# Kernel optimization log

Measured on AMD Instinct MI355X. Metric: run time of the kernel, lower is better.

Reference implementation:

```python
import jax, jax.numpy as jnp
import numpy as np

D_MODEL = 2048
N_HEADS = 16
HEAD_DIM = D_MODEL // N_HEADS
ROPE_BASE = 10000.0
B, T = 2, 2048


def setup_inputs() -> dict:
    key = jax.random.key(0)
    k1, k2, k3 = jax.random.split(key, 3)
    s_in = 1.0 / np.sqrt(D_MODEL)
    x = jax.random.normal(k1, (B, T, D_MODEL), dtype=jnp.float32)
    Wqkv = jax.random.normal(k2, (3 * D_MODEL, D_MODEL), dtype=jnp.float32) * s_in
    bqkv = jnp.zeros((3 * D_MODEL,), dtype=jnp.float32)
    Wo = jax.random.normal(k3, (D_MODEL, D_MODEL), dtype=jnp.float32) * s_in
    bo = jnp.zeros((D_MODEL,), dtype=jnp.float32)
    return {"x": x, "Wqkv": Wqkv, "bqkv": bqkv, "Wo": Wo, "bo": bo}


def _rotate_half(x):
    # [x1,x2,x3,x4] -> [-x2,x1,-x4,x3] (interleaved pairs)
    x_even = x[..., 0::2]
    x_odd = x[..., 1::2]
    return jnp.stack((-x_odd, x_even), axis=-1).reshape(x.shape)


def _rope_cos_sin(seq_len, dtype):
    half = HEAD_DIM // 2
    inv_freq = 1.0 / (ROPE_BASE ** (jnp.arange(half, dtype=jnp.float32) / half))
    freqs = jnp.arange(seq_len, dtype=jnp.float32)[:, None] * inv_freq[None, :]  # (T, half)
    emb = jnp.repeat(freqs, 2, axis=-1)  # (T, D) interleaved
    cos = jnp.cos(emb).astype(dtype)[None, None]  # (1,1,T,D)
    sin = jnp.sin(emb).astype(dtype)[None, None]
    return cos, sin


def reference(x, Wqkv, bqkv, Wo, bo):
    b, t, c = x.shape
    qkv = jnp.einsum('btc,fc->btf', x, Wqkv) + bqkv  # (B,T,3C)
    q, k, v = jnp.split(qkv, 3, axis=-1)
    def to_heads(z):
        return z.reshape(b, t, N_HEADS, HEAD_DIM).transpose(0, 2, 1, 3)  # (B,H,T,D)
    q, k, v = to_heads(q), to_heads(k), to_heads(v)
    cos, sin = _rope_cos_sin(t, x.dtype)
    q = q * cos + _rotate_half(q) * sin
    k = k * cos + _rotate_half(k) * sin
    scale = 1.0 / jnp.sqrt(jnp.asarray(HEAD_DIM, dtype=x.dtype))
    scores = jnp.einsum('bhqd,bhkd->bhqk', q, k) * scale  # (B,H,T,T)
    causal = jnp.tril(jnp.ones((t, t), dtype=bool))
    scores = jnp.where(causal, scores, jnp.finfo(scores.dtype).min)
    attn = jax.nn.softmax(scores, axis=-1)
    out = jnp.einsum('bhqk,bhkd->bhqd', attn, v)  # (B,H,T,D)
    out = out.transpose(0, 2, 1, 3).reshape(b, t, c)
    return jnp.einsum('btc,oc->bto', out, Wo) + bo
```

## Files before the change

kernel.cpp:

```cpp
#include <hip/hip_runtime.h>

using f16 = _Float16;
typedef _Float16 h8 __attribute__((ext_vector_type(8)));
typedef _Float16 h4 __attribute__((ext_vector_type(4)));
typedef float f4 __attribute__((ext_vector_type(4)));
typedef unsigned int u32;
typedef unsigned long long u64;

#define DEVI static __device__ __forceinline__

DEVI f4 mfma16(h8 a, h8 b, f4 c) {
  return __builtin_amdgcn_mfma_f32_16x16x32_f16(a, b, c, 0, 0, 0);
}

DEVI void gl_lds16(const f16* g, f16* l) {
  __builtin_amdgcn_global_load_lds(
      (const __attribute__((address_space(1))) u32*)g,
      (__attribute__((address_space(3))) u32*)l, 16, 0, 0);
}

DEVI u32 pkh2(float a, float b) {
  union { f16 h[2]; u32 u; } x;
  x.h[0] = (f16)a; x.h[1] = (f16)b;
  return x.u;
}

typedef float fv4 __attribute__((ext_vector_type(4)));

__global__ __launch_bounds__(256) void k_cvt(const float* __restrict__ in,
                                             f16* __restrict__ out, int n4) {
  int i = blockIdx.x * 256 + threadIdx.x;
  if (i >= n4) return;
  fv4 v = ((const fv4*)in)[i];
  h4 o;
  o[0] = (f16)v[0]; o[1] = (f16)v[1]; o[2] = (f16)v[2]; o[3] = (f16)v[3];
  ((h4*)out)[i] = o;
}

__global__ __launch_bounds__(256) void k_rope_tbl(float* __restrict__ tbl) {
  int i = blockIdx.x * 256 + threadIdx.x;
  int t = i >> 6, d = i & 63;
  float invf = exp2f(-(float)d * (13.287712379549449f / 64.f));
  float a = (float)t * invf;
  tbl[2 * i]     = cosf(a);
  tbl[2 * i + 1] = sinf(a);
}

template <int F32OUT>
__global__ __launch_bounds__(256) void k_gemm_bt(const f16* __restrict__ A,
                                                 const f16* __restrict__ Bt,
                                                 const float* __restrict__ bias,
                                                 void* __restrict__ Cp,
                                                 int M, int N, int K) {
  __shared__ f16 lds[2 * 128 * 64];
  f16* sA = lds;
  f16* sB = lds + 128 * 64;
  const int tid = threadIdx.x;
  const int w = tid >> 6, lane = tid & 63;
  const int g = lane >> 4, colq = lane & 15;
  const int wr = w >> 1, wc = w & 1;
  const int bm = blockIdx.y, bn = blockIdx.x;

  f4 acc[4][4] = {};
  const int nk = K >> 6;
  const int lrow = lane >> 3;
  const int lch = lane & 7;

  for (int k0i = 0; k0i < nk; ++k0i) {
    const int k0 = k0i << 6;
#pragma unroll
    for (int c = 0; c < 4; ++c) {
      const int seg = c * 4 + w;
      const int row = seg * 8 + lrow;
      const f16* ga = A + (size_t)(bm * 128 + row) * K + k0 + lch * 8;
      const f16* gb = Bt + (size_t)(bn * 128 + row) * K + k0 + lch * 8;
      gl_lds16(ga, sA + seg * 512);
      gl_lds16(gb, sB + seg * 512);
    }
    __syncthreads();
#pragma unroll
    for (int kk = 0; kk < 64; kk += 32) {
      h8 af[4], bf[4];
#pragma unroll
      for (int m = 0; m < 4; ++m)
        af[m] = *(const h8*)(sA + (wr * 64 + m * 16 + colq) * 64 + kk + g * 8);
#pragma unroll
      for (int n = 0; n < 4; ++n)
        bf[n] = *(const h8*)(sB + (wc * 64 + n * 16 + colq) * 64 + kk + g * 8);
#pragma unroll
      for (int m = 0; m < 4; ++m)
#pragma unroll
        for (int n = 0; n < 4; ++n) acc[m][n] = mfma16(af[m], bf[n], acc[m][n]);
    }
    __syncthreads();
  }

#pragma unroll
  for (int n = 0; n < 4; ++n) {
    const int col = bn * 128 + wc * 64 + n * 16 + colq;
    const float bv = bias[col];
#pragma unroll
    for (int m = 0; m < 4; ++m) {
      const int row0 = bm * 128 + wr * 64 + m * 16 + 4 * g;
#pragma unroll
      for (int r = 0; r < 4; ++r) {
        float v = acc[m][n][r] + bv;
        if constexpr (F32OUT) {
          ((float*)Cp)[(size_t)(row0 + r) * N + col] = v;
        } else {
          ((f16*)Cp)[(size_t)(row0 + r) * N + col] = (f16)v;
        }
      }
    }
  }
}

__global__ __launch_bounds__(256) void k_rope(const f16* __restrict__ qkv,
                                              const float* __restrict__ tbl,
                                              f16* __restrict__ Q, f16* __restrict__ K) {
  int i = blockIdx.x * 256 + threadIdx.x;
  int d = i & 63;
  int h = (i >> 6) & 15;
  int bt = i >> 10;
  int t = bt & 2047;
  int bh = ((bt >> 11) << 4) | h;
  union { u32 u; f16 h2[2]; } qa, ka, qo, ko;
  qa.u = *(const u32*)(qkv + (size_t)bt * 6144 + h * 128 + 2 * d);
  ka.u = *(const u32*)(qkv + (size_t)bt * 6144 + 2048 + h * 128 + 2 * d);
  float c = tbl[2 * (t * 64 + d)];
  float s = tbl[2 * (t * 64 + d) + 1];
  float q0f = (float)qa.h2[0], q1f = (float)qa.h2[1];
  float k0f = (float)ka.h2[0], k1f = (float)ka.h2[1];
  const float SQ = 0.088388347648318447f * 1.4426950408889634f;
  qo.h2[0] = (f16)((q0f * c - q1f * s) * SQ);
  qo.h2[1] = (f16)((q1f * c + q0f * s) * SQ);
  ko.h2[0] = (f16)(k0f * c - k1f * s);
  ko.h2[1] = (f16)(k1f * c + k0f * s);
  *(u32*)(Q + ((size_t)bh * 2048 + t) * 128 + 2 * d) = qo.u;
  *(u32*)(K + ((size_t)bh * 2048 + t) * 128 + 2 * d) = ko.u;
}

__global__ __launch_bounds__(256) void k_vtrans(const f16* __restrict__ qkv,
                                                f16* __restrict__ Vt) {
  __shared__ f16 ldsT[128 * 40];
  const int bh = blockIdx.y, t0 = blockIdx.x * 32;
  const int b = bh >> 4, h = bh & 15;
  const int tid = threadIdx.x;
#pragma unroll
  for (int cc = 0; cc < 2; ++cc) {
    int task = tid + cc * 256;
    int row = task >> 4;
    int ch = task & 15;
    h8 v = *(const h8*)(qkv + (size_t)(b * 2048 + t0 + row) * 6144 + 4096 + h * 128 + ch * 8);
#pragma unroll
    for (int j = 0; j < 8; ++j) ldsT[(ch * 8 + j) * 40 + row] = v[j];
  }
  __syncthreads();
  int d = tid >> 1, seg = tid & 1;
  h8 v0 = *(const h8*)(ldsT + d * 40 + seg * 16);
  h8 v1 = *(const h8*)(ldsT + d * 40 + seg * 16 + 8);
  f16* dst = Vt + ((size_t)bh * 128 + d) * 2048 + t0 + seg * 16;
  *(h8*)dst = v0;
  *(h8*)(dst + 8) = v1;
}

DEVI void stage_tiles(const f16* __restrict__ Kg, const f16* __restrict__ Vtg,
                      f16* bufK, f16* bufV, int kv, int w, int lane) {
#pragma unroll
  for (int jj = 0; jj < 4; ++jj) {
    const int j = w * 4 + jj;
    const int rK = j * 4 + (lane >> 4);
    const int cK = (lane & 15) ^ ((rK & 7) << 1);
    gl_lds16(Kg + (size_t)(kv + rK) * 128 + cK * 8, bufK + j * 512);
    const int rV = j * 8 + (lane >> 3);
    const int cV = (lane & 7) ^ (rV & 7);
    gl_lds16(Vtg + (size_t)rV * 2048 + kv + cV * 8, bufV + j * 512);
  }
}

__global__ __launch_bounds__(256, 1) void k_attn(const f16* __restrict__ Q,
                                                 const f16* __restrict__ K,
                                                 const f16* __restrict__ Vt,
                                                 f16* __restrict__ O) {
  __shared__ f16 lds[2][16384];
  const int tid = threadIdx.x;
  const int w = tid >> 6, lane = tid & 63;
  const int g = lane >> 4, q = lane & 15;
  const int bid = blockIdx.x;
  const int bh = bid & 31;
  const int b = bid >> 5;

  const f16* Kg = K + (size_t)bh * 2048 * 128;
  const f16* Vtg = Vt + (size_t)bh * 128 * 2048;
  const int qx2 = (q & 7) << 1;
  const int qx = q & 7;

  for (int ph = 0; ph < 2; ++ph) {
    const int p = ph ? (15 - b) : b;
    const int q0w = p * 128 + w * 32;
    const int nit = 2 * (p + 1);

    h8 qf[2][4];
#pragma unroll
    for (int set = 0; set < 2; ++set)
#pragma unroll
      for (int d4 = 0; d4 < 4; ++d4)
        qf[set][d4] = *(const h8*)(Q + ((size_t)bh * 2048 + q0w + 16 * set + q) * 128 + d4 * 32 + g * 8);

    stage_tiles(Kg, Vtg, lds[0], lds[0] + 8192, 0, w, lane);
    asm volatile("s_waitcnt vmcnt(0)" ::: "memory");
    __builtin_amdgcn_s_barrier();

    f4 ot[2][8] = {};
    float mrun[2] = {-3.0e38f, -3.0e38f};
    float lrun[2] = {0.f, 0.f};

    for (int it = 0; it < nit; ++it) {
      const int kv0 = it * 64;
      f16* bufK = lds[it & 1];
      f16* bufV = bufK + 8192;
      if (it + 1 < nit) {
        f16* nb = lds[(it + 1) & 1];
        stage_tiles(Kg, Vtg, nb, nb + 8192, kv0 + 64, w, lane);
      }
      if (kv0 < q0w + 32) {
        f4 st[2][4] = {{{0.f,0.f,0.f,0.f},{0.f,0.f,0.f,0.f},{0.f,0.f,0.f,0.f},{0.f,0.f,0.f,0.f}},
                       {{0.f,0.f,0.f,0.f},{0.f,0.f,0.f,0.f},{0.f,0.f,0.f,0.f},{0.f,0.f,0.f,0.f}}};
#pragma unroll
        for (int d4 = 0; d4 < 4; ++d4) {
          h8 kf[4];
#pragma unroll
          for (int s = 0; s < 4; ++s)
            kf[s] = *(const h8*)(bufK + ((16 * s + q) * 16 + ((4 * d4 + g) ^ qx2)) * 8);
#pragma unroll
          for (int set = 0; set < 2; ++set)
#pragma unroll
            for (int s = 0; s < 4; ++s)
              st[set][s] = mfma16(kf[s], qf[set][d4], st[set][s]);
        }
        if (kv0 + 63 > q0w) {
#pragma unroll
          for (int set = 0; set < 2; ++set) {
            const int qcol = q0w + 16 * set + q;
#pragma unroll
            for (int s = 0; s < 4; ++s)
#pragma unroll
              for (int r = 0; r < 4; ++r)
                if (kv0 + s * 16 + 4 * g + r > qcol) st[set][s][r] = -3.0e38f;
          }
        }
        float pm[2];
#pragma unroll
        for (int set = 0; set < 2; ++set) {
          float m0 = st[set][0][0];
#pragma unroll
          for (int s = 0; s < 4; ++s)
#pragma unroll
            for (int r = 0; r < 4; ++r) m0 = fmaxf(m0, st[set][s][r]);
          m0 = fmaxf(m0, __shfl_xor(m0, 16));
          m0 = fmaxf(m0, __shfl_xor(m0, 32));
          pm[set] = m0;
        }
        const bool ok = (pm[0] <= mrun[0] + 8.0f) && (pm[1] <= mrun[1] + 8.0f);
        if (!__all(ok)) {
#pragma unroll
          for (int set = 0; set < 2; ++set) {
            float mnew = fmaxf(mrun[set], pm[set]);
            float corr = exp2f(mrun[set] - mnew);
            lrun[set] *= corr;
#pragma unroll
            for (int dt = 0; dt < 8; ++dt) ot[set][dt] *= corr;
            mrun[set] = mnew;
          }
        }
#pragma unroll
        for (int set = 0; set < 2; ++set) {
          float ps = 0.f;
#pragma unroll
          for (int s = 0; s < 4; ++s)
#pragma unroll
            for (int r = 0; r < 4; ++r) {
              st[set][s][r] = exp2f(st[set][s][r] - mrun[set]);
              ps += st[set][s][r];
            }
          ps += __shfl_xor(ps, 16);
          ps += __shfl_xor(ps, 32);
          lrun[set] += ps;
        }
        union { u32 u[4]; h8 h; } pb[2][2];
        const int s0l = ((g & 1) << 5) | q;
        const bool hi = g >= 2;
#pragma unroll
        for (int set = 0; set < 2; ++set)
#pragma unroll
          for (int hh = 0; hh < 2; ++hh) {
            u32 wA0 = pkh2(st[set][2 * hh][0], st[set][2 * hh][1]);
            u32 wB0 = pkh2(st[set][2 * hh][2], st[set][2 * hh][3]);
            u32 wA1 = pkh2(st[set][2 * hh + 1][0], st[set][2 * hh + 1][1]);
            u32 wB1 = pkh2(st[set][2 * hh + 1][2], st[set][2 * hh + 1][3]);
            u32 a0 = (u32)__shfl((int)wA0, s0l),      a1 = (u32)__shfl((int)wA1, s0l);
            u32 b0 = (u32)__shfl((int)wB0, s0l),      b1 = (u32)__shfl((int)wB1, s0l);
            u32 c0 = (u32)__shfl((int)wA0, s0l + 16), c1 = (u32)__shfl((int)wA1, s0l + 16);
            u32 d0 = (u32)__shfl((int)wB0, s0l + 16), d1 = (u32)__shfl((int)wB1, s0l + 16);
            pb[set][hh].u[0] = hi ? a1 : a0;
            pb[set][hh].u[1] = hi ? b1 : b0;
            pb[set][hh].u[2] = hi ? c1 : c0;
            pb[set][hh].u[3] = hi ? d1 : d0;
          }
#pragma unroll
        for (int hh = 0; hh < 2; ++hh)
#pragma unroll
          for (int dt = 0; dt < 8; ++dt) {
            h8 vf = *(const h8*)(bufV + ((dt * 16 + q) * 8 + ((4 * hh + g) ^ qx)) * 8);
#pragma unroll
            for (int set = 0; set < 2; ++set)
              ot[set][dt] = mfma16(vf, pb[set][hh].h, ot[set][dt]);
          }
      }
      asm volatile("s_waitcnt vmcnt(0)" ::: "memory");
      __builtin_amdgcn_s_barrier();
    }

#pragma unroll
    for (int set = 0; set < 2; ++set) {
      float linv = 1.0f / lrun[set];
      f16* Ob = O + ((size_t)(bh >> 4) * 2048 + q0w + 16 * set + q) * 2048 + (bh & 15) * 128 + 4 * g;
#pragma unroll
      for (int dt = 0; dt < 8; ++dt) {
        union { f16 hh4[4]; u64 u; } o;
#pragma unroll
        for (int r = 0; r < 4; ++r) o.hh4[r] = (f16)(ot[set][dt][r] * linv);
        *(u64*)(Ob + dt * 16) = o.u;
      }
    }
  }
}

extern "C" void kernel_launch(void* const* d_in, const int* in_sizes, int n_in,
                              void* d_out, int out_size, void* d_ws, size_t ws_size,
                              hipStream_t stream) {
  (void)in_sizes; (void)n_in; (void)out_size; (void)ws_size;
  const float* x    = (const float*)d_in[0];
  const float* Wqkv = (const float*)d_in[1];
  const float* bqkv = (const float*)d_in[2];
  const float* Wo   = (const float*)d_in[3];
  const float* bo   = (const float*)d_in[4];

  char* ws = (char*)d_ws;
  f16* xb    = (f16*)ws; ws += (size_t)4096 * 2048 * 2;
  f16* wqkvb = (f16*)ws; ws += (size_t)6144 * 2048 * 2;
  f16* wob   = (f16*)ws; ws += (size_t)2048 * 2048 * 2;
  f16* qkvb  = (f16*)ws; ws += (size_t)4096 * 6144 * 2;
  f16* Qb    = (f16*)ws; ws += (size_t)32 * 2048 * 128 * 2;
  f16* Kb    = (f16*)ws; ws += (size_t)32 * 2048 * 128 * 2;
  f16* Vtb   = (f16*)ws; ws += (size_t)32 * 128 * 2048 * 2;
  f16* attb  = (f16*)ws; ws += (size_t)4096 * 2048 * 2;
  float* tbl = (float*)ws; ws += (size_t)2048 * 64 * 2 * 4;

  k_cvt<<<8192, 256, 0, stream>>>(x, xb, 2097152);
  k_cvt<<<12288, 256, 0, stream>>>(Wqkv, wqkvb, 3145728);
  k_cvt<<<4096, 256, 0, stream>>>(Wo, wob, 1048576);
  k_rope_tbl<<<512, 256, 0, stream>>>(tbl);

  k_gemm_bt<0><<<dim3(48, 32), 256, 0, stream>>>(xb, wqkvb, bqkv, qkvb, 4096, 6144, 2048);

  k_rope<<<16384, 256, 0, stream>>>(qkvb, tbl, Qb, Kb);
  k_vtrans<<<dim3(64, 32), 256, 0, stream>>>(qkvb, Vtb);

  k_attn<<<256, 256, 0, stream>>>(Qb, Kb, Vtb, attb);

  k_gemm_bt<1><<<dim3(16, 32), 256, 0, stream>>>(attb, wob, bo, d_out, 4096, 2048, 2048);
}
```

Baseline: 345.2 us.

## Rewrite projection GEMMs with 128x256 tiles, double-buffered LDS, swizzle and XCD remap

Replaces the simple single-buffered 128x128 GEMM with a 512-thread 128x256-tile kernel. It double-buffers LDS with async global->LDS loads and uses manual vmcnt waits so the next K tile is fetched while MFMAs run. It also XOR-swizzles LDS chunks to avoid bank conflicts, remaps block ids for XCD/L2 locality, and raises wave priority during MFMA. The risks are fewer blocks for the output GEMM (256 WGs), which may underfill the GPU, and a fragile manual waitcnt accounting.

```diff
diff --git a/kernel.cpp b/kernel.cpp
--- a/kernel.cpp
+++ b/kernel.cpp
@@ -47,57 +47,91 @@
 }
 
 template <int F32OUT>
-__global__ __launch_bounds__(256) void k_gemm_bt(const f16* __restrict__ A,
-                                                 const f16* __restrict__ Bt,
-                                                 const float* __restrict__ bias,
-                                                 void* __restrict__ Cp,
-                                                 int M, int N, int K) {
-  __shared__ f16 lds[2 * 128 * 64];
-  f16* sA = lds;
-  f16* sB = lds + 128 * 64;
+__global__ __launch_bounds__(512, 2) void k_gemm256(const f16* __restrict__ A,
+                                                    const f16* __restrict__ Bt,
+                                                    const float* __restrict__ bias,
+                                                    void* __restrict__ Cp,
+                                                    int M, int N, int K, int gy) {
+  __shared__ f16 lds[2][24576];
   const int tid = threadIdx.x;
   const int w = tid >> 6, lane = tid & 63;
   const int g = lane >> 4, colq = lane & 15;
-  const int wr = w >> 1, wc = w & 1;
-  const int bm = blockIdx.y, bn = blockIdx.x;
+  const int wr = w >> 2, wc = w & 3;
+
+  const int nwg = gridDim.x;
+  const int q8 = nwg >> 3;
+  const int swz = (blockIdx.x & 7) * q8 + (blockIdx.x >> 3);
+  const int bm = swz % gy, bn = swz / gy;
+
+  const f16* Ab = A + (size_t)bm * 128 * K;
+  const f16* Bb = Bt + (size_t)bn * 256 * K;
+
+  const int srow = lane >> 3;
+  const int schunk = (lane & 7) ^ srow;
+  const int nt = K >> 6;
+
+  auto STAGE = [&](int kt, f16* buf) {
+    const int k0 = kt << 6;
+    f16* bA = buf;
+    f16* bB = buf + 128 * 64;
+#pragma unroll
+    for (int j = 0; j < 2; ++j) {
+      const int r = w * 16 + j * 8;
+      gl_lds16(Ab + (size_t)(r + srow) * K + k0 + schunk * 8, bA + r * 64);
+    }
+#pragma unroll
+    for (int j = 0; j < 4; ++j) {
+      const int r = w * 32 + j * 8;
+      gl_lds16(Bb + (size_t)(r + srow) * K + k0 + schunk * 8, bB + r * 64);
+    }
+  };
+
+  STAGE(0, lds[0]);
+  STAGE(1, lds[1]);
+  asm volatile("s_waitcnt vmcnt(6)" ::: "memory");
+  __builtin_amdgcn_s_barrier();
 
   f4 acc[4][4] = {};
-  const int nk = K >> 6;
-  const int lrow = lane >> 3;
-  const int lch = lane & 7;
-
-  for (int k0i = 0; k0i < nk; ++k0i) {
-    const int k0 = k0i << 6;
-#pragma unroll
-    for (int c = 0; c < 4; ++c) {
-      const int seg = c * 4 + w;
-      const int row = seg * 8 + lrow;
-      const f16* ga = A + (size_t)(bm * 128 + row) * K + k0 + lch * 8;
-      const f16* gb = Bt + (size_t)(bn * 128 + row) * K + k0 + lch * 8;
-      gl_lds16(ga, sA + seg * 512);
-      gl_lds16(gb, sB + seg * 512);
-    }
-    __syncthreads();
-#pragma unroll
-    for (int kk = 0; kk < 64; kk += 32) {
-      h8 af[4], bf[4];
+  const int rowA0 = wr * 64 + colq;
+  const int rowB0 = wc * 64 + colq;
+  const int cq7 = colq & 7;
+
+  for (int t = 0; t < nt; ++t) {
+    f16* cur = lds[t & 1];
+    h8 af[2][4], bf[2][4];
+#pragma unroll
+    for (int kki = 0; kki < 2; ++kki) {
 #pragma unroll
       for (int m = 0; m < 4; ++m)
-        af[m] = *(const h8*)(sA + (wr * 64 + m * 16 + colq) * 64 + kk + g * 8);
+        af[kki][m] = *(const h8*)(cur + (rowA0 + m * 16) * 64 + (((kki * 4 + g) ^ cq7) * 8));
 #pragma unroll
       for (int n = 0; n < 4; ++n)
-        bf[n] = *(const h8*)(sB + (wc * 64 + n * 16 + colq) * 64 + kk + g * 8);
-#pragma unroll
-      for (int m = 0; m < 4; ++m)
-#pragma unroll
-        for (int n = 0; n < 4; ++n) acc[m][n] = mfma16(af[m], bf[n], acc[m][n]);
-    }
-    __syncthreads();
+        bf[kki][n] = *(const h8*)(cur + 8192 + (rowB0 + n * 16) * 64 + (((kki * 4 + g) ^ cq7) * 8));
+    }
+    asm volatile("s_waitcnt lgkmcnt(0)" ::: "memory");
+    __builtin_amdgcn_s_barrier();
+    const bool more = (t + 2 < nt);
+    if (more) STAGE(t + 2, cur);
+    __builtin_amdgcn_s_setprio(1);
+#pragma unroll
+    for (int m = 0; m < 4; ++m)
+#pragma unroll
+      for (int n = 0; n < 4; ++n)
+#pragma unroll
+        for (int kki = 0; kki < 2; ++kki)
+          acc[m][n] = mfma16(af[kki][m], bf[kki][n], acc[m][n]);
+    __builtin_amdgcn_s_setprio(0);
+    if (more) {
+      asm volatile("s_waitcnt vmcnt(6)" ::: "memory");
+    } else {
+      asm volatile("s_waitcnt vmcnt(0)" ::: "memory");
+    }
+    __builtin_amdgcn_s_barrier();
   }
 
 #pragma unroll
   for (int n = 0; n < 4; ++n) {
-    const int col = bn * 128 + wc * 64 + n * 16 + colq;
+    const int col = bn * 256 + wc * 64 + n * 16 + colq;
     const float bv = bias[col];
 #pragma unroll
     for (int m = 0; m < 4; ++m) {
@@ -362,12 +396,12 @@
   k_cvt<<<4096, 256, 0, stream>>>(Wo, wob, 1048576);
   k_rope_tbl<<<512, 256, 0, stream>>>(tbl);
 
-  k_gemm_bt<0><<<dim3(48, 32), 256, 0, stream>>>(xb, wqkvb, bqkv, qkvb, 4096, 6144, 2048);
+  k_gemm256<0><<<768, 512, 0, stream>>>(xb, wqkvb, bqkv, qkvb, 4096, 6144, 2048, 32);
 
   k_rope<<<16384, 256, 0, stream>>>(qkvb, tbl, Qb, Kb);
   k_vtrans<<<dim3(64, 32), 256, 0, stream>>>(qkvb, Vtb);
 
   k_attn<<<256, 256, 0, stream>>>(Qb, Kb, Vtb, attb);
 
-  k_gemm_bt<1><<<dim3(16, 32), 256, 0, stream>>>(attb, wob, bo, d_out, 4096, 2048, 2048);
-}
+  k_gemm256<1><<<256, 512, 0, stream>>>(attb, wob, bo, d_out, 4096, 2048, 2048, 32);
+}
```

Measured after the change: 317.9 us. 7.9% less time.
